# Optimization experiments

Measured on AMD Instinct MI355X. Metric: run time of the kernel, lower is better.

## Reference

```python
import jax, jax.numpy as jnp
import numpy as np

D_MODEL, D_STATE, N_HEADS = 1024, 64, 16


def setup_inputs() -> dict:
    key = jax.random.key(0)
    ks = jax.random.split(key, 4)
    B, T = 4, 4096
    s = 1.0 / np.sqrt(D_MODEL)
    x = jax.random.normal(ks[0], (B, T, D_MODEL), dtype=jnp.float32)
    h_prev = jnp.zeros((B, N_HEADS, D_STATE), dtype=jnp.float32)
    gate_w = jax.random.normal(ks[1], (2 * N_HEADS * D_STATE, D_MODEL), dtype=jnp.float32) * s
    # torch init: forget-gate bias = 1, input-gate bias = 0
    gate_b = jnp.concatenate([jnp.ones(N_HEADS * D_STATE), jnp.zeros(N_HEADS * D_STATE)]).astype(jnp.float32)
    value_w = jax.random.normal(ks[2], (N_HEADS * D_STATE, D_MODEL), dtype=jnp.float32) * s
    out_w = jax.random.normal(ks[3], (D_MODEL, N_HEADS * D_STATE), dtype=jnp.float32) * s
    return {"x": x, "h_prev": h_prev, "gate_w": gate_w, "gate_b": gate_b, "value_w": value_w, "out_w": out_w}


def reference(x, h_prev, gate_w, gate_b, value_w, out_w):
    B, T, _ = x.shape
    H, S = N_HEADS, D_STATE
    gates = (jnp.einsum('btd,gd->btg', x, gate_w) + gate_b).reshape(B, T, 2, H, S)
    A = jax.nn.sigmoid(gates[:, :, 0])   # [B,T,H,S] forget gate
    Bg = jax.nn.sigmoid(gates[:, :, 1])  # [B,T,H,S] input gate
    V = jnp.einsum('btd,vd->btv', x, value_w).reshape(B, T, H, S)

    def step(h, inp):
        a_t, bv_t = inp
        h = a_t * h + bv_t
        return h, h

    # time-major for scan; precompute B*V elementwise product
    a_tm = jnp.moveaxis(A, 1, 0)                # [T,B,H,S]
    bv_tm = jnp.moveaxis(Bg * V, 1, 0)          # [T,B,H,S]
    h_last, h_seq = jax.lax.scan(step, h_prev, (a_tm, bv_tm))
    h_flat = jnp.moveaxis(h_seq, 0, 1).reshape(B, T, H * S)
    y = jnp.einsum('btv,dv->btd', h_flat, out_w)  # dropout is identity at p=0/eval
    return y, h_last
```

## Files before the change

### kernel.cpp

```cpp
#include <hip/hip_runtime.h>
#include <cstdint>
#include <cstddef>


typedef _Float16 f16;
typedef _Float16 f16x2 __attribute__((ext_vector_type(2)));
typedef _Float16 f16x8 __attribute__((ext_vector_type(8)));
typedef float    f32x4 __attribute__((ext_vector_type(4)));

__device__ __forceinline__ void gload_lds16(const void* g, void* l) {
  __builtin_amdgcn_global_load_lds(
      (const __attribute__((address_space(1))) void*)g,
      (__attribute__((address_space(3))) void*)l, 16, 0, 0);
}

__device__ __forceinline__ float sigmoidf_(float x) {
  return 1.0f / (1.0f + __expf(-x));
}

__global__ __launch_bounds__(256) void cast_pack(
    const float* __restrict__ x, const float* __restrict__ gw,
    const float* __restrict__ vw, const float* __restrict__ ow,
    f16* __restrict__ xh, f16* __restrict__ wgv, f16* __restrict__ owb) {
  const int XG = 2097152, GG = 262144, VG = 131072, OG = 131072;
  int id = blockIdx.x * 256 + threadIdx.x;
  const float* src;
  f16* dst;
  if (id < XG) {
    src = x + (size_t)id * 8;
    dst = xh + (size_t)id * 8;
  } else if (id < XG + GG) {
    int g = id - XG;
    int row = g >> 7, col = g & 127;
    int drow = (row < 1024) ? row : (1024 + 2 * (row - 1024));
    src = gw + ((size_t)row << 10) + col * 8;
    dst = wgv + ((size_t)drow << 10) + col * 8;
  } else if (id < XG + GG + VG) {
    int g = id - XG - GG;
    int row = g >> 7, col = g & 127;
    int drow = 1024 + 2 * row + 1;
    src = vw + ((size_t)row << 10) + col * 8;
    dst = wgv + ((size_t)drow << 10) + col * 8;
  } else if (id < XG + GG + VG + OG) {
    int g = id - XG - GG - VG;
    src = ow + (size_t)g * 8;
    dst = owb + (size_t)g * 8;
  } else {
    return;
  }
  float4 v0 = ((const float4*)src)[0], v1 = ((const float4*)src)[1];
  f16x8 o;
  o[0] = (f16)v0.x; o[1] = (f16)v0.y; o[2] = (f16)v0.z; o[3] = (f16)v0.w;
  o[4] = (f16)v1.x; o[5] = (f16)v1.y; o[6] = (f16)v1.z; o[7] = (f16)v1.w;
  *(f16x8*)dst = o;
}

template <int EPI>
__global__ __launch_bounds__(256, 3) void gemm_bt(
    const f16* __restrict__ A, const f16* __restrict__ Bw,
    const float* __restrict__ gate_b,
    void* __restrict__ o0v, void* __restrict__ o1v) {
  constexpr int K = 1024;
  __shared__ __align__(16) f16 S[17920];
  f16* As = S;
  f16* Bs = S + 8192;
  const int tid  = threadIdx.x;
  const int lane = tid & 63;
  const int quad = lane >> 4;
  const int wv   = tid >> 6;
  const int wrow = wv & 1, wcol = wv >> 1;
  const int n0 = blockIdx.y * 128;
  const int m0 = blockIdx.x * 128;

  const f16* ga[4];
  const f16* gb[4];
  f16* la[4];
  f16* lb[4];
#pragma unroll
  for (int j = 0; j < 4; ++j) {
    int s   = j * 256 + tid;
    int row = s >> 3;
    int kc  = (s & 7) ^ (row & 7);
    ga[j] = A  + (size_t)(n0 + row) * K + kc * 8;
    gb[j] = Bw + (size_t)(m0 + row) * K + kc * 8;
    la[j] = &As[s * 8];
    lb[j] = &Bs[s * 8];
  }

  f32x4 acc[4][4];
#pragma unroll
  for (int mi = 0; mi < 4; ++mi)
#pragma unroll
    for (int ni = 0; ni < 4; ++ni) acc[mi][ni] = (f32x4){0.f, 0.f, 0.f, 0.f};

  for (int k0 = 0; k0 < K; k0 += 64) {
#pragma unroll
    for (int j = 0; j < 4; ++j) gload_lds16(ga[j], la[j]);
#pragma unroll
    for (int j = 0; j < 4; ++j) gload_lds16(gb[j], lb[j]);
#pragma unroll
    for (int j = 0; j < 4; ++j) { ga[j] += 64; gb[j] += 64; }
    __syncthreads();
#pragma unroll
    for (int kk = 0; kk < 2; ++kk) {
      f16x8 af[4], bfv[4];
#pragma unroll
      for (int mi = 0; mi < 4; ++mi) {
        int row  = wrow * 64 + mi * 16 + (lane & 15);
        int slot = row * 8 + ((kk * 4 + quad) ^ (row & 7));
        af[mi] = *(const f16x8*)(&As[slot * 8]);
      }
#pragma unroll
      for (int ni = 0; ni < 4; ++ni) {
        int row  = wcol * 64 + ni * 16 + (lane & 15);
        int slot = row * 8 + ((kk * 4 + quad) ^ (row & 7));
        bfv[ni] = *(const f16x8*)(&Bs[slot * 8]);
      }
#pragma unroll
      for (int mi = 0; mi < 4; ++mi)
#pragma unroll
        for (int ni = 0; ni < 4; ++ni)
          acc[mi][ni] = __builtin_amdgcn_mfma_f32_16x16x32_f16(
              af[mi], bfv[ni], acc[mi][ni], 0, 0, 0);
    }
    __syncthreads();
  }

  if (EPI == 1) {
#pragma unroll
    for (int mi = 0; mi < 4; ++mi)
#pragma unroll
      for (int ni = 0; ni < 4; ++ni) {
        const int m = m0 + wcol * 64 + ni * 16 + (lane & 15);
#pragma unroll
        for (int r = 0; r < 4; ++r) {
          const int n = n0 + wrow * 64 + mi * 16 + quad * 4 + r;
          ((float*)o0v)[(size_t)n * 1024 + m] = acc[mi][ni][r];
        }
      }
    return;
  }

  if (m0 < 1024) {
#pragma unroll
    for (int mi = 0; mi < 4; ++mi)
#pragma unroll
      for (int ni = 0; ni < 4; ++ni) {
        const int ml = wcol * 64 + ni * 16 + (lane & 15);
#pragma unroll
        for (int r = 0; r < 4; ++r) {
          const int nl = wrow * 64 + mi * 16 + quad * 4 + r;
          S[nl * 136 + ml] = (f16)sigmoidf_(acc[mi][ni][r] + gate_b[m0 + ml]);
        }
      }
    __syncthreads();
    f16* o0 = (f16*)o0v;
#pragma unroll
    for (int i = 0; i < 8; ++i) {
      int ch = i * 256 + tid;
      int row = ch >> 4, cc = ch & 15;
      f16x8 vv = *(const f16x8*)&S[row * 136 + cc * 8];
      *(f16x8*)(o0 + (size_t)(n0 + row) * 1024 + m0 + cc * 8) = vv;
    }
  } else {
    const int c0 = (m0 - 1024) >> 1;
#pragma unroll
    for (int mi = 0; mi < 4; ++mi)
#pragma unroll
      for (int ni = 0; ni < 4; ++ni) {
        const int ml = wcol * 64 + ni * 16 + (lane & 15);
#pragma unroll
        for (int r = 0; r < 4; ++r) {
          float val = acc[mi][ni][r];
          float pv = __shfl_xor(val, 1, 64);
          if (!(lane & 1)) {
            const int c = ml >> 1;
            const int nl = wrow * 64 + mi * 16 + quad * 4 + r;
            S[nl * 72 + c] =
                (f16)(sigmoidf_(val + gate_b[1024 + c0 + c]) * pv);
          }
        }
      }
    __syncthreads();
    f16* o1 = (f16*)o1v;
#pragma unroll
    for (int i = 0; i < 4; ++i) {
      int ch = i * 256 + tid;
      int row = ch >> 3, cc = ch & 7;
      f16x8 vv = *(const f16x8*)&S[row * 72 + cc * 8];
      *(f16x8*)(o1 + (size_t)(n0 + row) * 1024 + c0 + cc * 8) = vv;
    }
  }
}

__global__ __launch_bounds__(256) void scan_pass1(
    const f16x2* __restrict__ a, const f16x2* __restrict__ bv,
    float2* __restrict__ Ac, float2* __restrict__ Uc) {
  const int c2 = blockIdx.x * 256 + threadIdx.x;
  const int j = blockIdx.y;
  const int b = blockIdx.z;
  const size_t base = ((size_t)(b * 4096 + j * 32)) * 512 + c2;
  float P0 = 1.f, P1 = 1.f, U0 = 0.f, U1 = 0.f;
#pragma unroll 8
  for (int t = 0; t < 32; ++t) {
    const size_t o = base + (size_t)t * 512;
    f16x2 at = a[o], bt = bv[o];
    float a0 = (float)at[0], a1 = (float)at[1];
    P0 *= a0; P1 *= a1;
    U0 = a0 * U0 + (float)bt[0];
    U1 = a1 * U1 + (float)bt[1];
  }
  const size_t o = ((size_t)(b * 128 + j)) * 512 + c2;
  Ac[o] = make_float2(P0, P1);
  Uc[o] = make_float2(U0, U1);
}

__global__ __launch_bounds__(256) void scan_pass2(
    const float* __restrict__ Ac, const float* __restrict__ Uc,
    const float* __restrict__ h_prev, float* __restrict__ Hs,
    float* __restrict__ hlast) {
  const int id = blockIdx.x * 256 + threadIdx.x;
  const int b = id >> 10, c = id & 1023;
  float H = h_prev[b * 1024 + c];
  for (int j = 0; j < 128; ++j) {
    const size_t o = ((size_t)(b * 128 + j)) * 1024 + c;
    Hs[o] = H;
    H = Ac[o] * H + Uc[o];
  }
  hlast[b * 1024 + c] = H;
}

__global__ __launch_bounds__(256) void scan_pass3(
    const f16x2* __restrict__ a, const f16x2* __restrict__ bv,
    const float2* __restrict__ Hs, f16x2* __restrict__ hb) {
  const int c2 = blockIdx.x * 256 + threadIdx.x;
  const int j = blockIdx.y;
  const int b = blockIdx.z;
  const size_t base = ((size_t)(b * 4096 + j * 32)) * 512 + c2;
  float2 H = Hs[((size_t)(b * 128 + j)) * 512 + c2];
  float h0 = H.x, h1 = H.y;
#pragma unroll 8
  for (int t = 0; t < 32; ++t) {
    const size_t o = base + (size_t)t * 512;
    f16x2 at = a[o], bt = bv[o];
    h0 = (float)at[0] * h0 + (float)bt[0];
    h1 = (float)at[1] * h1 + (float)bt[1];
    f16x2 hv; hv[0] = (f16)h0; hv[1] = (f16)h1;
    hb[o] = hv;
  }
}

extern "C" void kernel_launch(void* const* d_in, const int* in_sizes, int n_in,
                              void* d_out, int out_size, void* d_ws,
                              size_t ws_size, hipStream_t stream) {
  const float* x       = (const float*)d_in[0];
  const float* h_prev  = (const float*)d_in[1];
  const float* gate_w  = (const float*)d_in[2];
  const float* gate_b  = (const float*)d_in[3];
  const float* value_w = (const float*)d_in[4];
  const float* out_w   = (const float*)d_in[5];
  float* out = (float*)d_out;

  char* ws = (char*)d_ws;
  f16*   xh   = (f16*)(ws);
  f16*   wgv  = (f16*)(ws + 33554432);
  f16*   owb  = (f16*)(ws + 39845888);
  f16*   abuf = (f16*)(ws + 41943040);
  f16*   bvb  = (f16*)(ws + 75497472);
  float* Ac   = (float*)(ws + 109051904);
  float* Uc   = (float*)(ws + 111149056);
  float* Hs   = (float*)(ws + 113246208);
  float* hlast = out + 16777216;

  cast_pack<<<10240, 256, 0, stream>>>(x, gate_w, value_w, out_w, xh, wgv,
                                       owb);

  gemm_bt<0><<<dim3(24, 128), 256, 0, stream>>>(xh, wgv, gate_b, abuf, bvb);

  scan_pass1<<<dim3(2, 128, 4), 256, 0, stream>>>(
      (const f16x2*)abuf, (const f16x2*)bvb, (float2*)Ac, (float2*)Uc);
  scan_pass2<<<16, 256, 0, stream>>>(Ac, Uc, h_prev, Hs, hlast);
  scan_pass3<<<dim3(2, 128, 4), 256, 0, stream>>>(
      (const f16x2*)abuf, (const f16x2*)bvb, (const float2*)Hs, (f16x2*)xh);

  gemm_bt<1><<<dim3(8, 128), 256, 0, stream>>>(xh, owb, nullptr, out, nullptr);
}
```

Measured before the change: 373.3 us.

## Use 32x32x16 MFMA in GEMMs and parallelize chunk-carry scan across segments

Result: faster. 360.5 us (-3.4%).

```diff
diff --git a/kernel.cpp b/kernel.cpp
--- a/kernel.cpp
+++ b/kernel.cpp
@@ -6,7 +6,7 @@
 typedef _Float16 f16;
 typedef _Float16 f16x2 __attribute__((ext_vector_type(2)));
 typedef _Float16 f16x8 __attribute__((ext_vector_type(8)));
-typedef float    f32x4 __attribute__((ext_vector_type(4)));
+typedef float    f32x16 __attribute__((ext_vector_type(16)));
 
 __device__ __forceinline__ void gload_lds16(const void* g, void* l) {
   __builtin_amdgcn_global_load_lds(
@@ -66,7 +66,8 @@
   f16* Bs = S + 8192;
   const int tid  = threadIdx.x;
   const int lane = tid & 63;
-  const int quad = lane >> 4;
+  const int half = lane >> 5;
+  const int l31  = lane & 31;
   const int wv   = tid >> 6;
   const int wrow = wv & 1, wcol = wv >> 1;
   const int n0 = blockIdx.y * 128;
@@ -87,11 +88,13 @@
     lb[j] = &Bs[s * 8];
   }
 
-  f32x4 acc[4][4];
-#pragma unroll
-  for (int mi = 0; mi < 4; ++mi)
-#pragma unroll
-    for (int ni = 0; ni < 4; ++ni) acc[mi][ni] = (f32x4){0.f, 0.f, 0.f, 0.f};
+  f32x16 acc[2][2];
+#pragma unroll
+  for (int mi = 0; mi < 2; ++mi)
+#pragma unroll
+    for (int ni = 0; ni < 2; ++ni)
+#pragma unroll
+      for (int e = 0; e < 16; ++e) acc[mi][ni][e] = 0.f;
 
   for (int k0 = 0; k0 < K; k0 += 64) {
 #pragma unroll
@@ -102,25 +105,25 @@
     for (int j = 0; j < 4; ++j) { ga[j] += 64; gb[j] += 64; }
     __syncthreads();
 #pragma unroll
-    for (int kk = 0; kk < 2; ++kk) {
-      f16x8 af[4], bfv[4];
-#pragma unroll
-      for (int mi = 0; mi < 4; ++mi) {
-        int row  = wrow * 64 + mi * 16 + (lane & 15);
-        int slot = row * 8 + ((kk * 4 + quad) ^ (row & 7));
+    for (int kk = 0; kk < 4; ++kk) {
+      f16x8 af[2], bfv[2];
+#pragma unroll
+      for (int mi = 0; mi < 2; ++mi) {
+        int row  = wrow * 64 + mi * 32 + l31;
+        int slot = row * 8 + ((kk * 2 + half) ^ (row & 7));
         af[mi] = *(const f16x8*)(&As[slot * 8]);
       }
 #pragma unroll
-      for (int ni = 0; ni < 4; ++ni) {
-        int row  = wcol * 64 + ni * 16 + (lane & 15);
-        int slot = row * 8 + ((kk * 4 + quad) ^ (row & 7));
+      for (int ni = 0; ni < 2; ++ni) {
+        int row  = wcol * 64 + ni * 32 + l31;
+        int slot = row * 8 + ((kk * 2 + half) ^ (row & 7));
         bfv[ni] = *(const f16x8*)(&Bs[slot * 8]);
       }
 #pragma unroll
-      for (int mi = 0; mi < 4; ++mi)
-#pragma unroll
-        for (int ni = 0; ni < 4; ++ni)
-          acc[mi][ni] = __builtin_amdgcn_mfma_f32_16x16x32_f16(
+      for (int mi = 0; mi < 2; ++mi)
+#pragma unroll
+        for (int ni = 0; ni < 2; ++ni)
+          acc[mi][ni] = __builtin_amdgcn_mfma_f32_32x32x16_f16(
               af[mi], bfv[ni], acc[mi][ni], 0, 0, 0);
     }
     __syncthreads();
@@ -128,13 +131,14 @@
 
   if (EPI == 1) {
 #pragma unroll
-    for (int mi = 0; mi < 4; ++mi)
-#pragma unroll
-      for (int ni = 0; ni < 4; ++ni) {
-        const int m = m0 + wcol * 64 + ni * 16 + (lane & 15);
-#pragma unroll
-        for (int r = 0; r < 4; ++r) {
-          const int n = n0 + wrow * 64 + mi * 16 + quad * 4 + r;
+    for (int mi = 0; mi < 2; ++mi)
+#pragma unroll
+      for (int ni = 0; ni < 2; ++ni) {
+        const int m = m0 + wcol * 64 + ni * 32 + l31;
+#pragma unroll
+        for (int r = 0; r < 16; ++r) {
+          const int n = n0 + wrow * 64 + mi * 32 + (r & 3) + 8 * (r >> 2) +
+                        4 * half;
           ((float*)o0v)[(size_t)n * 1024 + m] = acc[mi][ni][r];
         }
       }
@@ -143,14 +147,16 @@
 
   if (m0 < 1024) {
 #pragma unroll
-    for (int mi = 0; mi < 4; ++mi)
-#pragma unroll
-      for (int ni = 0; ni < 4; ++ni) {
-        const int ml = wcol * 64 + ni * 16 + (lane & 15);
-#pragma unroll
-        for (int r = 0; r < 4; ++r) {
-          const int nl = wrow * 64 + mi * 16 + quad * 4 + r;
-          S[nl * 136 + ml] = (f16)sigmoidf_(acc[mi][ni][r] + gate_b[m0 + ml]);
+    for (int mi = 0; mi < 2; ++mi)
+#pragma unroll
+      for (int ni = 0; ni < 2; ++ni) {
+        const int ml = wcol * 64 + ni * 32 + l31;
+        const float bias = gate_b[m0 + ml];
+#pragma unroll
+        for (int r = 0; r < 16; ++r) {
+          const int nl = wrow * 64 + mi * 32 + (r & 3) + 8 * (r >> 2) +
+                         4 * half;
+          S[nl * 136 + ml] = (f16)sigmoidf_(acc[mi][ni][r] + bias);
         }
       }
     __syncthreads();
@@ -165,17 +171,18 @@
   } else {
     const int c0 = (m0 - 1024) >> 1;
 #pragma unroll
-    for (int mi = 0; mi < 4; ++mi)
-#pragma unroll
-      for (int ni = 0; ni < 4; ++ni) {
-        const int ml = wcol * 64 + ni * 16 + (lane & 15);
-#pragma unroll
-        for (int r = 0; r < 4; ++r) {
+    for (int mi = 0; mi < 2; ++mi)
+#pragma unroll
+      for (int ni = 0; ni < 2; ++ni) {
+        const int ml = wcol * 64 + ni * 32 + l31;
+#pragma unroll
+        for (int r = 0; r < 16; ++r) {
           float val = acc[mi][ni][r];
           float pv = __shfl_xor(val, 1, 64);
           if (!(lane & 1)) {
             const int c = ml >> 1;
-            const int nl = wrow * 64 + mi * 16 + quad * 4 + r;
+            const int nl = wrow * 64 + mi * 32 + (r & 3) + 8 * (r >> 2) +
+                           4 * half;
             S[nl * 72 + c] =
                 (f16)(sigmoidf_(val + gate_b[1024 + c0 + c]) * pv);
           }
@@ -219,15 +226,37 @@
     const float* __restrict__ Ac, const float* __restrict__ Uc,
     const float* __restrict__ h_prev, float* __restrict__ Hs,
     float* __restrict__ hlast) {
-  const int id = blockIdx.x * 256 + threadIdx.x;
-  const int b = id >> 10, c = id & 1023;
-  float H = h_prev[b * 1024 + c];
-  for (int j = 0; j < 128; ++j) {
+  __shared__ float SA[4][64], SU[4][64];
+  const int tid = threadIdx.x;
+  const int seg = tid >> 6;
+  const int cl  = tid & 63;
+  const int ch  = blockIdx.x * 64 + cl;
+  const int b = ch >> 10, c = ch & 1023;
+  float A = 1.f, U = 0.f;
+  for (int t = 0; t < 32; ++t) {
+    const int j = seg * 32 + t;
+    const size_t o = ((size_t)(b * 128 + j)) * 1024 + c;
+    float av = Ac[o], uv = Uc[o];
+    U = av * U + uv;
+    A = av * A;
+  }
+  SA[seg][cl] = A;
+  SU[seg][cl] = U;
+  __syncthreads();
+  float Ae = 1.f, Ue = 0.f;
+  for (int s = 0; s < seg; ++s) {
+    float av = SA[s][cl], uv = SU[s][cl];
+    Ue = av * Ue + uv;
+    Ae = av * Ae;
+  }
+  float H = Ae * h_prev[b * 1024 + c] + Ue;
+  for (int t = 0; t < 32; ++t) {
+    const int j = seg * 32 + t;
     const size_t o = ((size_t)(b * 128 + j)) * 1024 + c;
     Hs[o] = H;
     H = Ac[o] * H + Uc[o];
   }
-  hlast[b * 1024 + c] = H;
+  if (seg == 3) hlast[b * 1024 + c] = H;
 }
 
 __global__ __launch_bounds__(256) void scan_pass3(
@@ -279,7 +308,7 @@
 
   scan_pass1<<<dim3(2, 128, 4), 256, 0, stream>>>(
       (const f16x2*)abuf, (const f16x2*)bvb, (float2*)Ac, (float2*)Uc);
-  scan_pass2<<<16, 256, 0, stream>>>(Ac, Uc, h_prev, Hs, hlast);
+  scan_pass2<<<64, 256, 0, stream>>>(Ac, Uc, h_prev, Hs, hlast);
   scan_pass3<<<dim3(2, 128, 4), 256, 0, stream>>>(
       (const f16x2*)abuf, (const f16x2*)bvb, (const float2*)Hs, (f16x2*)xh);
 
```
